# Performance work log

Measured on AMD Instinct MI355X. Metric: run time of the kernel, lower is better.

## Reference

```python
import jax, jax.numpy as jnp
import numpy as np

B, L, H = 8, 2048, 1024
MASK_IDENTITY = True


def setup_inputs() -> dict:
    key = jax.random.key(0)
    ks = jax.random.split(key, 7)
    s = 1.0 / np.sqrt(H)
    return {
        "x": jax.random.normal(ks[0], (B, L, H), dtype=jnp.float32),
        "Wq": jax.random.uniform(ks[1], (H, H), jnp.float32, -s, s),
        "bq": jax.random.uniform(ks[2], (H,), jnp.float32, -s, s),
        "Wk": jax.random.uniform(ks[3], (H, H), jnp.float32, -s, s),
        "bk": jax.random.uniform(ks[4], (H,), jnp.float32, -s, s),
        "Wv": jax.random.uniform(ks[5], (H, H), jnp.float32, -s, s),
        "bv": jax.random.uniform(ks[6], (H,), jnp.float32, -s, s),
    }


def reference(x, Wq, bq, Wk, bk, Wv, bv):
    # Linear layers (torch Linear: y = x @ W.T + b)
    q = jnp.einsum("blh,oh->blo", x, Wq) + bq
    k = jnp.einsum("blh,oh->blo", x, Wk) + bk
    v = jnp.einsum("blh,oh->blo", x, Wv) + bv
    hidden = q.shape[-1]
    # NOTE: original scales by hidden_size, not sqrt(hidden_size)
    attn = jnp.einsum("blh,bmh->blm", q / hidden, k)  # [B, L, L]
    if MASK_IDENTITY:
        mask_value = -jnp.finfo(attn.dtype).max
        eye = jnp.eye(attn.shape[-1], dtype=bool)  # [L, L]
        attn = jnp.where(eye[None, :, :], mask_value, attn)
    attn = jax.nn.softmax(attn, axis=-1)
    return jnp.einsum("blm,bmh->blh", attn, v)
```

## Files before the change

### kernel.cpp

```cpp
#include <hip/hip_runtime.h>


typedef unsigned short u16;
typedef __bf16 bfx8 __attribute__((ext_vector_type(8)));
typedef float f32x4 __attribute__((ext_vector_type(4)));

__device__ __forceinline__ u16 f2bf(float f) {
    unsigned int x = __float_as_uint(f);
    unsigned int r = (x + 0x7fffu + ((x >> 16) & 1u)) >> 16;
    return (u16)r;
}
__device__ __forceinline__ float bf2f(u16 u) {
    return __uint_as_float(((unsigned int)u) << 16);
}

__global__ void f32_to_bf16(const float* __restrict__ src, u16* __restrict__ dst, int n8) {
    int i = blockIdx.x * blockDim.x + threadIdx.x;
    if (i < n8) {
        float4 a = ((const float4*)src)[i * 2];
        float4 b = ((const float4*)src)[i * 2 + 1];
        ushort4 lo; lo.x = f2bf(a.x); lo.y = f2bf(a.y); lo.z = f2bf(a.z); lo.w = f2bf(a.w);
        ushort4 hi; hi.x = f2bf(b.x); hi.y = f2bf(b.y); hi.z = f2bf(b.z); hi.w = f2bf(b.w);
        ((ushort4*)dst)[i * 2] = lo;
        ((ushort4*)dst)[i * 2 + 1] = hi;
    }
}

__global__ void transpose_bf16(const u16* __restrict__ src, u16* __restrict__ dst) {
    __shared__ u16 s[64][64 + 8];
    int z = blockIdx.z;
    int tm = blockIdx.x * 64;
    int th = blockIdx.y * 64;
    const u16* sp = src + (long)z * 2048 * 1024;
    u16* dp = dst + (long)z * 1024 * 2048;
    int t = threadIdx.x;
#pragma unroll
    for (int p = 0; p < 4; ++p) {
        int r = p * 16 + (t >> 4);
        int c = (t & 15) * 4;
        ushort4 v = *(const ushort4*)(sp + (long)(tm + r) * 1024 + th + c);
        s[r][c] = v.x; s[r][c + 1] = v.y; s[r][c + 2] = v.z; s[r][c + 3] = v.w;
    }
    __syncthreads();
#pragma unroll
    for (int p = 0; p < 4; ++p) {
        int hr = p * 16 + (t >> 4);
        int c = (t & 15) * 4;
        ushort4 v;
        v.x = s[c][hr]; v.y = s[c + 1][hr]; v.z = s[c + 2][hr]; v.w = s[c + 3][hr];
        *(ushort4*)(dp + (long)(th + hr) * 2048 + tm + c) = v;
    }
}


#define FENCE asm volatile("" ::: "memory")
#define BAR   __builtin_amdgcn_s_barrier()
#define PRIO1 __builtin_amdgcn_s_setprio(1)
#define PRIO0 __builtin_amdgcn_s_setprio(0)

#define STAGEF(DST, SRC, LD, tt) do{ \
    _Pragma("unroll") \
    for (int rnd = 0; rnd < 4; ++rnd) { \
        int c_ = rnd * 512 + tid; \
        int row_ = c_ >> 3; \
        int slot_ = c_ & 7; \
        const u16* g_ = (SRC) + (long)row_ * (LD) + (tt) * 64 + ((slot_ ^ (row_ & 7)) << 3); \
        char* l_ = (char*)(DST) + rnd * 8192 + wid * 1024; \
        __builtin_amdgcn_global_load_lds((__attribute__((address_space(1))) void*)g_, \
            (__attribute__((address_space(3))) void*)l_, 16, 0, 0); \
    } \
}while(0)

#define RD_A4(dst, SARR, mibase) do{ \
    const char* _b = (const char*)(SARR) + ((wr * 128 + (mibase) * 16 + rA) * 128); \
    dst[0][0] = *(const bfx8*)(_b + 0 * 2048 + ofk0); dst[0][1] = *(const bfx8*)(_b + 0 * 2048 + ofk1); \
    dst[1][0] = *(const bfx8*)(_b + 1 * 2048 + ofk0); dst[1][1] = *(const bfx8*)(_b + 1 * 2048 + ofk1); \
    dst[2][0] = *(const bfx8*)(_b + 2 * 2048 + ofk0); dst[2][1] = *(const bfx8*)(_b + 2 * 2048 + ofk1); \
    dst[3][0] = *(const bfx8*)(_b + 3 * 2048 + ofk0); dst[3][1] = *(const bfx8*)(_b + 3 * 2048 + ofk1); \
}while(0)

#define RD_B2(dst, SARR, nibase) do{ \
    const char* _b = (const char*)(SARR) + ((wc * 64 + (nibase) * 16 + rA) * 128); \
    dst[0][0] = *(const bfx8*)(_b + 0 * 2048 + ofk0); dst[0][1] = *(const bfx8*)(_b + 0 * 2048 + ofk1); \
    dst[1][0] = *(const bfx8*)(_b + 1 * 2048 + ofk0); dst[1][1] = *(const bfx8*)(_b + 1 * 2048 + ofk1); \
}while(0)

#define MMQ(AS, BS, M0, N0) do{ \
    _Pragma("unroll") \
    for (int ks = 0; ks < 2; ++ks) \
    _Pragma("unroll") \
    for (int mi = 0; mi < 4; ++mi) \
    _Pragma("unroll") \
    for (int ni = 0; ni < 2; ++ni) \
        acc[(M0)+mi][(N0)+ni] = __builtin_amdgcn_mfma_f32_16x16x32_bf16(AS[mi][ks], BS[ni][ks], acc[(M0)+mi][(N0)+ni], 0, 0, 0); \
}while(0)

#define TILE(SA_R, SB_R, SA_O, tt) do{ \
     \
    RD_B2(b01, SB_R, 0); RD_B2(b23, SB_R, 2); \
    FENCE; BAR; PRIO1; MMQ(aA, b01, 0, 0); PRIO0; FENCE; BAR; \
     \
    RD_A4(aB, SA_R, 4); \
    FENCE; BAR; PRIO1; MMQ(aA, b23, 0, 2); PRIO0; FENCE; BAR; \
     \
    asm volatile("s_waitcnt vmcnt(0)" ::: "memory"); \
    if ((tt) + 2 < NT) STAGEF(SB_R, B, ldb, (tt) + 2); \
    FENCE; BAR; PRIO1; MMQ(aB, b23, 4, 2); PRIO0; FENCE; BAR; \
     \
    RD_A4(aA, SA_O, 0); \
    if ((tt) + 2 < NT) STAGEF(SA_R, A, lda, (tt) + 2); \
    FENCE; BAR; PRIO1; MMQ(aB, b01, 4, 0); PRIO0; FENCE; BAR; \
}while(0)

template <int MODE>
__global__ __launch_bounds__(512, 2) void gemm8p(
    const u16* __restrict__ Ab, const u16* __restrict__ Bb,
    int K, int lda, int ldb,
    long strideA, long strideB,
    const float* __restrict__ biasCat,
    u16* __restrict__ outBf, long strideP,
    float* __restrict__ den,
    float* __restrict__ outF)
{
    __shared__ __align__(16) u16 sA0[16384];
    __shared__ __align__(16) u16 sB0[16384];
    __shared__ __align__(16) u16 sA1[16384];
    __shared__ __align__(16) u16 sB1[16384];

    const int tid  = threadIdx.x;
    const int lane = tid & 63;
    const int wid  = tid >> 6;
    const int wr = wid >> 2, wc = wid & 3;
    const int z = blockIdx.z;
    const u16* A = Ab + (long)z * strideA + (long)blockIdx.x * 256 * lda;
    const u16* B = Bb + (long)z * strideB + (long)blockIdx.y * 256 * ldb;
    const int NT = K >> 6;

    const int rA  = lane & 15;
    const int cg  = lane >> 4;
    const int swz = rA & 7;
    const int ofk0 = ((cg)     ^ swz) << 4;
    const int ofk1 = ((cg | 4) ^ swz) << 4;

    f32x4 acc[8][4] = {};
    bfx8 aA[4][2], aB[4][2], b01[2][2], b23[2][2];

    STAGEF(sA0, A, lda, 0); STAGEF(sB0, B, ldb, 0);
    STAGEF(sA1, A, lda, 1); STAGEF(sB1, B, ldb, 1);
    asm volatile("s_waitcnt vmcnt(8)" ::: "memory");
    BAR;
    RD_A4(aA, sA0, 0);
    FENCE;

    for (int t = 0; t < NT; t += 2) {
        TILE(sA0, sB0, sA1, t);
        TILE(sA1, sB1, sA0, t + 1);
    }

    const int r0 = blockIdx.x * 256 + wr * 128 + (cg << 2);
    const int c0 = blockIdx.y * 256 + wc * 64 + rA;
#pragma unroll
    for (int mi = 0; mi < 8; ++mi) {
#pragma unroll
        for (int r = 0; r < 4; ++r) {
            const int grow = r0 + mi * 16 + r;
            if constexpr (MODE == 0) {
#pragma unroll
                for (int ni = 0; ni < 4; ++ni) {
                    int gcol = c0 + ni * 16;
                    float v = acc[mi][ni][r] + biasCat[gcol];
                    if (gcol < 1024) v *= (1.0f / 1024.0f);
                    int which = gcol >> 10;
                    long dst = (long)which * (16384L * 1024) + (long)grow * 1024 + (gcol & 1023);
                    outBf[dst] = f2bf(v);
                }
            } else if constexpr (MODE == 1) {
                float s = 0.0f;
#pragma unroll
                for (int ni = 0; ni < 4; ++ni) {
                    int gcol = c0 + ni * 16;
                    float p = (grow == gcol) ? 0.0f : __expf(acc[mi][ni][r]);
                    u16 pb = f2bf(p);
                    outBf[(long)z * strideP + (long)grow * 2048 + gcol] = pb;
                    s += bf2f(pb);
                }
                s += __shfl_xor(s, 1); s += __shfl_xor(s, 2);
                s += __shfl_xor(s, 4); s += __shfl_xor(s, 8);
                if (rA == 0) atomicAdd(&den[z * 2048 + grow], s);
            } else {
                float d = den[z * 2048 + grow];
#pragma unroll
                for (int ni = 0; ni < 4; ++ni)
                    outF[(long)z * (2048L * 1024) + (long)grow * 1024 + (c0 + ni * 16)] = acc[mi][ni][r] / d;
            }
        }
    }
}

extern "C" void kernel_launch(void* const* d_in, const int* in_sizes, int n_in,
                              void* d_out, int out_size, void* d_ws, size_t ws_size,
                              hipStream_t stream) {
    const float* x  = (const float*)d_in[0];
    const float* Wq = (const float*)d_in[1];
    const float* bq = (const float*)d_in[2];
    const float* Wk = (const float*)d_in[3];
    const float* bk = (const float*)d_in[4];
    const float* Wv = (const float*)d_in[5];
    const float* bv = (const float*)d_in[6];
    float* out = (float*)d_out;

    const long XB_OFF   = 0;
    const long WB_OFF   = 33554432;
    const long BIAS_OFF = WB_OFF + 6291456;
    const long DEN_OFF  = BIAS_OFF + 12288;
    const long QKV_OFF  = DEN_OFF + 65536;
    const long PB_OFF   = QKV_OFF + 2L * 33554432;
    const unsigned long long NEED = (unsigned long long)(PB_OFF + 67108864);
    if (ws_size < NEED) return;

    char* ws = (char*)d_ws;
    u16*   xb      = (u16*)(ws + XB_OFF);
    u16*   vT      = (u16*)(ws + XB_OFF);
    u16*   Wb      = (u16*)(ws + WB_OFF);
    float* biasCat = (float*)(ws + BIAS_OFF);
    float* den     = (float*)(ws + DEN_OFF);
    u16*   qkv     = (u16*)(ws + QKV_OFF);
    u16*   qb = qkv;
    u16*   kb = qkv + 16384L * 1024;
    u16*   vb = qkv + 2L * 16384 * 1024;
    u16*   Pb = (u16*)(ws + PB_OFF);

    f32_to_bf16<<<8192, 256, 0, stream>>>(x, xb, 2097152);
    f32_to_bf16<<<512, 256, 0, stream>>>(Wq, Wb, 131072);
    f32_to_bf16<<<512, 256, 0, stream>>>(Wk, Wb + 1048576, 131072);
    f32_to_bf16<<<512, 256, 0, stream>>>(Wv, Wb + 2097152, 131072);
    hipMemcpyAsync(biasCat,        bq, 4096, hipMemcpyDeviceToDevice, stream);
    hipMemcpyAsync(biasCat + 1024, bk, 4096, hipMemcpyDeviceToDevice, stream);
    hipMemcpyAsync(biasCat + 2048, bv, 4096, hipMemcpyDeviceToDevice, stream);
    hipMemsetAsync(den, 0, 65536, stream);

    gemm8p<0><<<dim3(64, 12, 1), 512, 0, stream>>>(
        xb, Wb, 1024, 1024, 1024, 0, 0, biasCat, qkv, 0, nullptr, nullptr);

    transpose_bf16<<<dim3(32, 16, 8), 256, 0, stream>>>(vb, vT);

    gemm8p<1><<<dim3(8, 8, 8), 512, 0, stream>>>(
        qb, kb, 1024, 1024, 1024, 2048L * 1024, 2048L * 1024,
        nullptr, Pb, 2048L * 2048, den, nullptr);

    gemm8p<2><<<dim3(8, 4, 8), 512, 0, stream>>>(
        Pb, vT, 2048, 2048, 2048, 2048L * 2048, 1024L * 2048,
        nullptr, nullptr, 0, den, out);
}
```

Measured before the change: 406.7 us.

## Split global-to-LDS staging into halves and interleave with MFMA phases

Global-to-LDS prefetch is now issued in half-tile chunks spread across the four MFMA phases of each tile. B for the next tile is staged one step ahead instead of two, and A stays two steps ahead. The full vmcnt(0) drain is replaced by partial waits (vmcnt 6 and 4), so memory traffic overlaps compute more evenly. The tighter prefetch distance for B and the hand-tuned wait counts risk stalls, or races if the counts are wrong.

Result: no change. 413.8 us (+1.7%).

```diff
diff --git a/kernel.cpp b/kernel.cpp
--- a/kernel.cpp
+++ b/kernel.cpp
@@ -57,15 +57,16 @@
 #define BAR   __builtin_amdgcn_s_barrier()
 #define PRIO1 __builtin_amdgcn_s_setprio(1)
 #define PRIO0 __builtin_amdgcn_s_setprio(0)
-
-#define STAGEF(DST, SRC, LD, tt) do{ \
-    _Pragma("unroll") \
-    for (int rnd = 0; rnd < 4; ++rnd) { \
+#define VMC(N) asm volatile("s_waitcnt vmcnt(" #N ")" ::: "memory")
+
+#define STAGE_HALF(DST, SRC, LD, tt, h) do{ \
+    _Pragma("unroll") \
+    for (int rnd = 0; rnd < 2; ++rnd) { \
         int c_ = rnd * 512 + tid; \
-        int row_ = c_ >> 3; \
+        int row_ = (h) * 128 + (c_ >> 3); \
         int slot_ = c_ & 7; \
         const u16* g_ = (SRC) + (long)row_ * (LD) + (tt) * 64 + ((slot_ ^ (row_ & 7)) << 3); \
-        char* l_ = (char*)(DST) + rnd * 8192 + wid * 1024; \
+        char* l_ = (char*)(DST) + (h) * 16384 + rnd * 8192 + wid * 1024; \
         __builtin_amdgcn_global_load_lds((__attribute__((address_space(1))) void*)g_, \
             (__attribute__((address_space(3))) void*)l_, 16, 0, 0); \
     } \
@@ -95,20 +96,23 @@
         acc[(M0)+mi][(N0)+ni] = __builtin_amdgcn_mfma_f32_16x16x32_bf16(AS[mi][ks], BS[ni][ks], acc[(M0)+mi][(N0)+ni], 0, 0, 0); \
 }while(0)
 
-#define TILE(SA_R, SB_R, SA_O, tt) do{ \
-     \
-    RD_B2(b01, SB_R, 0); RD_B2(b23, SB_R, 2); \
+#define TILE(SA_c, SB_c, SA_o, SB_o, tt) do{ \
+     \
+    RD_B2(b01, SB_c, 0); RD_B2(b23, SB_c, 2); \
+    if ((tt) + 1 < NT) STAGE_HALF(SB_o, B, ldb, (tt) + 1, 0); \
     FENCE; BAR; PRIO1; MMQ(aA, b01, 0, 0); PRIO0; FENCE; BAR; \
      \
-    RD_A4(aB, SA_R, 4); \
+    RD_A4(aB, SA_c, 4); \
+    if ((tt) + 1 < NT) STAGE_HALF(SB_o, B, ldb, (tt) + 1, 1); \
     FENCE; BAR; PRIO1; MMQ(aA, b23, 0, 2); PRIO0; FENCE; BAR; \
      \
-    asm volatile("s_waitcnt vmcnt(0)" ::: "memory"); \
-    if ((tt) + 2 < NT) STAGEF(SB_R, B, ldb, (tt) + 2); \
+    if ((tt) + 2 < NT) STAGE_HALF(SA_c, A, lda, (tt) + 2, 0); \
+    VMC(6); \
     FENCE; BAR; PRIO1; MMQ(aB, b23, 4, 2); PRIO0; FENCE; BAR; \
      \
-    RD_A4(aA, SA_O, 0); \
-    if ((tt) + 2 < NT) STAGEF(SA_R, A, lda, (tt) + 2); \
+    RD_A4(aA, SA_o, 0); \
+    if ((tt) + 2 < NT) STAGE_HALF(SA_c, A, lda, (tt) + 2, 1); \
+    VMC(4); \
     FENCE; BAR; PRIO1; MMQ(aB, b01, 4, 0); PRIO0; FENCE; BAR; \
 }while(0)
 
@@ -145,16 +149,17 @@
     f32x4 acc[8][4] = {};
     bfx8 aA[4][2], aB[4][2], b01[2][2], b23[2][2];
 
-    STAGEF(sA0, A, lda, 0); STAGEF(sB0, B, ldb, 0);
-    STAGEF(sA1, A, lda, 1); STAGEF(sB1, B, ldb, 1);
-    asm volatile("s_waitcnt vmcnt(8)" ::: "memory");
+    STAGE_HALF(sA0, A, lda, 0, 0); STAGE_HALF(sA0, A, lda, 0, 1);
+    STAGE_HALF(sB0, B, ldb, 0, 0); STAGE_HALF(sB0, B, ldb, 0, 1);
+    STAGE_HALF(sA1, A, lda, 1, 0); STAGE_HALF(sA1, A, lda, 1, 1);
+    VMC(4);
     BAR;
     RD_A4(aA, sA0, 0);
     FENCE;
 
     for (int t = 0; t < NT; t += 2) {
-        TILE(sA0, sB0, sA1, t);
-        TILE(sA1, sB1, sA0, t + 1);
+        TILE(sA0, sB0, sA1, sB1, t);
+        TILE(sA1, sB1, sA0, sB0, t + 1);
     }
 
     const int r0 = blockIdx.x * 256 + wr * 128 + (cg << 2);
```
